# Optimization experiments

Measured on AMD Instinct MI355X. Metric: run time of the kernel, lower is better.

## Reference

```python
import jax, jax.numpy as jnp
import numpy as np

IN_FEATURES = 4096
OUT_FEATURES = 4096
GROUP_SIZE = 128


def _unpack_int4_last_dim(packed):
    # packed: [..., P] int32 -> [..., P*8] int32 nibbles in [0,15]
    shifts = jnp.arange(0, 32, 4, dtype=jnp.int32)
    u = (packed[..., None] >> shifts) & 15
    return u.reshape(*packed.shape[:-1], packed.shape[-1] * 8)


def setup_inputs() -> dict:
    key = jax.random.key(0)
    k1, k2, k3, k4, k5 = jax.random.split(key, 5)
    groups = IN_FEATURES // GROUP_SIZE  # 32
    x = jax.random.normal(k1, (4096, IN_FEATURES), dtype=jnp.float32)
    qweight = jax.random.randint(k2, (OUT_FEATURES, IN_FEATURES // 8), 0, 2147483647, dtype=jnp.int32)
    qzeros = jax.random.randint(k3, (OUT_FEATURES, groups // 8), 0, 2147483647, dtype=jnp.int32)
    scales = jax.random.uniform(k4, (OUT_FEATURES, groups), dtype=jnp.float32) * 0.02 + 0.001
    bias = jax.random.normal(k5, (OUT_FEATURES,), dtype=jnp.float32)
    return {"x": x, "qweight": qweight, "qzeros": qzeros, "scales": scales, "bias": bias}


def _dequantize_weight(qweight, qzeros, scales):
    # qweight: [out, in/8] -> w_int: [out, in]
    w_int = _unpack_int4_last_dim(qweight).astype(jnp.float32)
    # qzeros: [out, groups/8] -> zeros: [out, groups]
    zeros = _unpack_int4_last_dim(qzeros).astype(jnp.float32)
    group_ids = jnp.arange(IN_FEATURES) // GROUP_SIZE  # [in]
    # expand per-group scale/zero along in_features
    w = (w_int - zeros[:, group_ids]) * scales[:, group_ids]  # [out, in]
    return w


def reference(x, qweight, qzeros, scales, bias):
    w = _dequantize_weight(qweight, qzeros, scales)  # [out, in] fp32
    return x @ w.T + bias  # [tokens, out]
```

## Files before the change

kernel.cpp:

```cpp
#include <hip/hip_runtime.h>
#include <hip/hip_bf16.h>

#define TOKENS 4096
#define IN_F   4096
#define OUT_F  4096

typedef __bf16 bf16x8 __attribute__((ext_vector_type(8)));
typedef float  f32x4  __attribute__((ext_vector_type(4)));
typedef unsigned int u32;
typedef u32 u32x4 __attribute__((ext_vector_type(4)));

#define DEQ_BLOCKS 2048
#define CVT_BLOCKS 4096

__device__ __forceinline__ void gld_lds16(const void* g, void* l) {
    __builtin_amdgcn_global_load_lds(
        (const __attribute__((address_space(1))) u32*)g,
        (__attribute__((address_space(3))) u32*)l,
        16, 0, 0);
}

__global__ __launch_bounds__(256) void prep_kernel(
        const u32* __restrict__ qweight, const u32* __restrict__ qzeros,
        const float* __restrict__ scales, const float* __restrict__ x,
        __bf16* __restrict__ W, __bf16* __restrict__ A) {
    const int tid = threadIdx.x;
    if (blockIdx.x < DEQ_BLOCKS) {
        int idx4 = blockIdx.x * 256 + tid;
        int n  = idx4 >> 7;
        int p4 = (idx4 & 127) << 2;
        int g  = p4 >> 4;
        u32 qz = qzeros[(n << 2) + (g >> 3)];
        float z = (float)((qz >> ((g & 7) * 4)) & 15);
        float s = scales[(n << 5) + g];
        u32x4 qw = *(const u32x4*)(qweight + (size_t)n * 512 + p4);
        __bf16* dst = W + (size_t)n * IN_F + p4 * 8;
#pragma unroll
        for (int c = 0; c < 4; ++c) {
            bf16x8 h;
#pragma unroll
            for (int j = 0; j < 8; ++j) {
                float w = ((float)((qw[c] >> (4 * j)) & 15) - z) * s;
                h[j] = (__bf16)w;
            }
            *(bf16x8*)(dst + c * 8) = h;
        }
    } else {
        int idx = (blockIdx.x - DEQ_BLOCKS) * 256 + tid;
        const f32x4* xp = (const f32x4*)x + (size_t)idx * 4;
        f32x4 v0 = xp[0], v1 = xp[1], v2 = xp[2], v3 = xp[3];
        bf16x8 h0, h1;
#pragma unroll
        for (int j = 0; j < 4; ++j) {
            h0[j] = (__bf16)v0[j]; h0[4 + j] = (__bf16)v1[j];
            h1[j] = (__bf16)v2[j]; h1[4 + j] = (__bf16)v3[j];
        }
        bf16x8* ap = (bf16x8*)A + (size_t)idx * 2;
        ap[0] = h0; ap[1] = h1;
    }
}

__global__ __launch_bounds__(512, 2) void gemm8p(
        const __bf16* __restrict__ A, const __bf16* __restrict__ B,
        const float* __restrict__ bias, float* __restrict__ C) {
    __shared__ __align__(16) char lsA[65536];
    __shared__ __align__(16) char lsB[65536];

    const int t    = threadIdx.x;
    const int lane = t & 63, wave = t >> 6;
    const int lr   = lane & 15, quad = lane >> 4;
    const int wm   = (wave >> 2) * 128;
    const int wn   = (wave & 3) * 64;

    int bid = blockIdx.x;
    bid = (bid & 7) * 32 + (bid >> 3);
    const int bm = bid >> 4, bn = bid & 15;

    const __bf16* Abase = A + (size_t)bm * 256 * IN_F;
    const __bf16* Bbase = B + (size_t)bn * 256 * IN_F;

    const int srow0 = t >> 2;
    const int srow1 = 128 + (t >> 2);
    const int scol0 = ((t & 3) ^ ((srow0 >> 1) & 3)) * 8;
    const int scol1 = ((t & 3) ^ ((srow1 >> 1) & 3)) * 8;

#define STAGE(OPBASE, LS, KT, KH, BUF) do {                                  \
    int _kb = (((KT) & 63) * 64 + (KH) * 32);                                \
    gld_lds16(OPBASE + (size_t)srow0 * IN_F + _kb + scol0,                   \
              LS + ((BUF) * 2 + (KH)) * 16384 + t * 16);                     \
    gld_lds16(OPBASE + (size_t)srow1 * IN_F + _kb + scol1,                   \
              LS + ((BUF) * 2 + (KH)) * 16384 + 8192 + t * 16);              \
} while (0)

    bf16x8 af[4], bfr[4];
    f32x4 acc[8][4] = {};

#define LDA4(PM, KH, BUF) do {                                               \
    _Pragma("unroll")                                                        \
    for (int i = 0; i < 4; ++i) {                                            \
        const int R = wm + (PM) * 64 + i * 16 + lr;                          \
        af[i] = *(const bf16x8*)(lsA + ((BUF) * 2 + (KH)) * 16384 +          \
                                 R * 64 + ((quad ^ ((R >> 1) & 3)) * 16));   \
    }                                                                        \
} while (0)

#define LDB4(KH, BUF) do {                                                   \
    _Pragma("unroll")                                                        \
    for (int j = 0; j < 4; ++j) {                                            \
        const int R = wn + j * 16 + lr;                                      \
        bfr[j] = *(const bf16x8*)(lsB + ((BUF) * 2 + (KH)) * 16384 +         \
                                  R * 64 + ((quad ^ ((R >> 1) & 3)) * 16));  \
    }                                                                        \
} while (0)

#define MFMA16(PM) do {                                                      \
    _Pragma("unroll")                                                        \
    for (int i = 0; i < 4; ++i)                                              \
    _Pragma("unroll")                                                        \
    for (int j = 0; j < 4; ++j)                                              \
        acc[(PM) * 4 + i][j] = __builtin_amdgcn_mfma_f32_16x16x32_bf16(      \
            af[i], bfr[j], acc[(PM) * 4 + i][j], 0, 0, 0);                   \
} while (0)

#define FENCE() asm volatile("" ::: "memory")
#define BAR()  do { FENCE(); __builtin_amdgcn_s_barrier(); FENCE(); } while (0)
#define VM8()  asm volatile("s_waitcnt vmcnt(8)" ::: "memory")
#define PRIO(x) __builtin_amdgcn_s_setprio(x)

    STAGE(Abase, lsA, 0, 0, 0);
    STAGE(Bbase, lsB, 0, 0, 0);
    STAGE(Abase, lsA, 0, 1, 0);
    STAGE(Bbase, lsB, 0, 1, 0);
    STAGE(Abase, lsA, 1, 0, 1);
    STAGE(Bbase, lsB, 1, 0, 1);
    VM8();
    BAR();

#define TILE(KT, B) do {                                                     \
       \
    LDB4(0, B); LDA4(0, 0, B);                                               \
    STAGE(Abase, lsA, (KT) + 1, 1, 1 - (B));                                 \
    BAR(); PRIO(1); MFMA16(0); PRIO(0); BAR();                               \
                        \
    LDA4(1, 0, B);                                                           \
    STAGE(Bbase, lsB, (KT) + 1, 1, 1 - (B));                                 \
    BAR(); PRIO(1); MFMA16(1); PRIO(0); VM8(); BAR();                        \
        \
    LDB4(1, B); LDA4(0, 1, B);                                               \
    STAGE(Abase, lsA, (KT) + 2, 0, B);                                       \
    BAR(); PRIO(1); MFMA16(0); PRIO(0); BAR();                               \
                                         \
    LDA4(1, 1, B);                                                           \
    STAGE(Bbase, lsB, (KT) + 2, 0, B);                                       \
    BAR(); PRIO(1); MFMA16(1); PRIO(0); VM8(); BAR();                        \
} while (0)

    for (int kt = 0; kt < 64; kt += 2) {
        TILE(kt, 0);
        TILE(kt + 1, 1);
    }

    asm volatile("s_waitcnt vmcnt(0)" ::: "memory");

    const int row0 = bm * 256 + wm + quad * 4;
    const int col0 = bn * 256 + wn + lr;
#pragma unroll
    for (int j = 0; j < 4; ++j) {
        const int col = col0 + j * 16;
        const float bv = bias[col];
#pragma unroll
        for (int i = 0; i < 8; ++i) {
            const int row = row0 + i * 16;
#pragma unroll
            for (int r = 0; r < 4; ++r)
                C[(size_t)(row + r) * OUT_F + col] = acc[i][j][r] + bv;
        }
    }
}

extern "C" void kernel_launch(void* const* d_in, const int* in_sizes, int n_in,
                              void* d_out, int out_size, void* d_ws, size_t ws_size,
                              hipStream_t stream) {
    (void)in_sizes; (void)n_in; (void)out_size; (void)ws_size;
    const float* x       = (const float*)d_in[0];
    const u32*   qweight = (const u32*)d_in[1];
    const u32*   qzeros  = (const u32*)d_in[2];
    const float* scales  = (const float*)d_in[3];
    const float* bias    = (const float*)d_in[4];
    float* out = (float*)d_out;

    __bf16* W   = (__bf16*)d_ws;
    __bf16* Abf = (__bf16*)((char*)d_ws + (size_t)OUT_F * IN_F * 2);

    prep_kernel<<<dim3(DEQ_BLOCKS + CVT_BLOCKS), dim3(256), 0, stream>>>(
        qweight, qzeros, scales, x, W, Abf);
    gemm8p<<<dim3(256), dim3(512), 0, stream>>>(Abf, W, bias, out);
}
```

Before: 257.8 us.

## Use inline-asm LDS reads with immediate offsets and restructure waitcnt schedule

Replaces compiler-generated LDS fragment loads with inline ds_read_b128 using a precomputed per-lane base and constant immediate offsets, removing per-load address arithmetic. Adds explicit lgkmcnt(0) waits plus sched_barrier after the barrier before each MFMA block. Changes the global-load wait from vmcnt(8) twice per tile to vmcnt(4) once per tile, altering how many prefetch loads stay in flight. This risks correctness if the swizzle simplification (using lr instead of full row) or the reduced waits mismatch the staging order, and may reduce latency hiding.

```diff
diff --git a/kernel.cpp b/kernel.cpp
--- a/kernel.cpp
+++ b/kernel.cpp
@@ -92,25 +92,34 @@
               LS + ((BUF) * 2 + (KH)) * 16384 + 8192 + t * 16);              \
 } while (0)
 
+    const u32 slot16 = (u32)((quad ^ ((lr >> 1) & 3)) * 16);
+    const u32 lsA0 = (u32)(size_t)(__attribute__((address_space(3))) char*)lsA;
+    const u32 lsB0 = (u32)(size_t)(__attribute__((address_space(3))) char*)lsB;
+    const u32 aA = lsA0 + (u32)((wm + lr) * 64) + slot16;
+    const u32 aB = lsB0 + (u32)((wn + lr) * 64) + slot16;
+
     bf16x8 af[4], bfr[4];
     f32x4 acc[8][4] = {};
 
+#define DSR(dst, base, OFF) do {                                             \
+    u32x4 _r;                                                                \
+    asm volatile("ds_read_b128 %0, %1 offset:%2"                             \
+                 : "=v"(_r) : "v"(base), "n"(OFF));                          \
+    dst = __builtin_bit_cast(bf16x8, _r);                                    \
+} while (0)
+
 #define LDA4(PM, KH, BUF) do {                                               \
-    _Pragma("unroll")                                                        \
-    for (int i = 0; i < 4; ++i) {                                            \
-        const int R = wm + (PM) * 64 + i * 16 + lr;                          \
-        af[i] = *(const bf16x8*)(lsA + ((BUF) * 2 + (KH)) * 16384 +          \
-                                 R * 64 + ((quad ^ ((R >> 1) & 3)) * 16));   \
-    }                                                                        \
+    DSR(af[0], aA, (((BUF)*2+(KH))*16384 + (PM)*4096 + 0*1024));             \
+    DSR(af[1], aA, (((BUF)*2+(KH))*16384 + (PM)*4096 + 1*1024));             \
+    DSR(af[2], aA, (((BUF)*2+(KH))*16384 + (PM)*4096 + 2*1024));             \
+    DSR(af[3], aA, (((BUF)*2+(KH))*16384 + (PM)*4096 + 3*1024));             \
 } while (0)
 
 #define LDB4(KH, BUF) do {                                                   \
-    _Pragma("unroll")                                                        \
-    for (int j = 0; j < 4; ++j) {                                            \
-        const int R = wn + j * 16 + lr;                                      \
-        bfr[j] = *(const bf16x8*)(lsB + ((BUF) * 2 + (KH)) * 16384 +         \
-                                  R * 64 + ((quad ^ ((R >> 1) & 3)) * 16));  \
-    }                                                                        \
+    DSR(bfr[0], aB, (((BUF)*2+(KH))*16384 + 0*1024));                        \
+    DSR(bfr[1], aB, (((BUF)*2+(KH))*16384 + 1*1024));                        \
+    DSR(bfr[2], aB, (((BUF)*2+(KH))*16384 + 2*1024));                        \
+    DSR(bfr[3], aB, (((BUF)*2+(KH))*16384 + 3*1024));                        \
 } while (0)
 
 #define MFMA16(PM) do {                                                      \
@@ -124,8 +133,11 @@
 
 #define FENCE() asm volatile("" ::: "memory")
 #define BAR()  do { FENCE(); __builtin_amdgcn_s_barrier(); FENCE(); } while (0)
-#define VM8()  asm volatile("s_waitcnt vmcnt(8)" ::: "memory")
+#define VM4()  asm volatile("s_waitcnt vmcnt(4)" ::: "memory")
 #define PRIO(x) __builtin_amdgcn_s_setprio(x)
+#define OPENB() do { BAR();                                                  \
+    asm volatile("s_waitcnt lgkmcnt(0)" ::: "memory");                       \
+    __builtin_amdgcn_sched_barrier(0); } while (0)
 
     STAGE(Abase, lsA, 0, 0, 0);
     STAGE(Bbase, lsB, 0, 0, 0);
@@ -133,26 +145,26 @@
     STAGE(Bbase, lsB, 0, 1, 0);
     STAGE(Abase, lsA, 1, 0, 1);
     STAGE(Bbase, lsB, 1, 0, 1);
-    VM8();
+    VM4();
     BAR();
 
 #define TILE(KT, B) do {                                                     \
-       \
+                          \
     LDB4(0, B); LDA4(0, 0, B);                                               \
     STAGE(Abase, lsA, (KT) + 1, 1, 1 - (B));                                 \
-    BAR(); PRIO(1); MFMA16(0); PRIO(0); BAR();                               \
+    OPENB(); PRIO(1); MFMA16(0); PRIO(0); BAR();                             \
                         \
     LDA4(1, 0, B);                                                           \
     STAGE(Bbase, lsB, (KT) + 1, 1, 1 - (B));                                 \
-    BAR(); PRIO(1); MFMA16(1); PRIO(0); VM8(); BAR();                        \
+    OPENB(); PRIO(1); MFMA16(1); PRIO(0); BAR();                             \
         \
     LDB4(1, B); LDA4(0, 1, B);                                               \
     STAGE(Abase, lsA, (KT) + 2, 0, B);                                       \
-    BAR(); PRIO(1); MFMA16(0); PRIO(0); BAR();                               \
-                                         \
+    OPENB(); PRIO(1); MFMA16(0); PRIO(0); BAR();                             \
+              \
     LDA4(1, 1, B);                                                           \
     STAGE(Bbase, lsB, (KT) + 2, 0, B);                                       \
-    BAR(); PRIO(1); MFMA16(1); PRIO(0); VM8(); BAR();                        \
+    OPENB(); PRIO(1); MFMA16(1); PRIO(0); VM4(); BAR();                      \
 } while (0)
 
     for (int kt = 0; kt < 64; kt += 2) {
```

New measurement: 247.5 us. 1.04x faster.
